# Kernel tuning notes

Measured on AMD Instinct MI355X. Metric: run time of the kernel, lower is better.

The kernel has to match this reference:

```python
import jax, jax.numpy as jnp
import numpy as np

B, T, H, A = 16, 6000, 256, 1
NOTE_CLS = 104            # note_num + 4
NOTE_NUM, NOTE_START = 100, 30
THRESHOLD = 0.5
MIN_GAP = 9


def conv1d(x, w, b):
    # x: [B,T,C], w: [K,Cin,Cout] (kernel 3, padding 1 == SAME)
    return jax.lax.conv_general_dilated(x, w, (1,), 'SAME', dimension_numbers=('NWC', 'WIO', 'NWC')) + b


def layer_norm(x, g, b, eps=1e-5):
    m = jnp.mean(x, -1, keepdims=True)
    v = jnp.mean((x - m) ** 2, -1, keepdims=True)
    return (x - m) * jax.lax.rsqrt(v + eps) * g + b


def regulate_boundary(bd_logits, non_padding):
    # threshold -> per-run local argmax -> min-gap NMS merge, sequential per row
    probs = jax.nn.sigmoid(bd_logits)          # [B,T]
    bd = probs > THRESHOLD
    Tn = probs.shape[1]

    def one_row(bd_i, p_i):
        def step(carry, j):
            res, start, last, best_i, best_v = carry
            is_one, pj = bd_i[j], p_i[j]
            opening = is_one & (start < 0)
            # running argmax over current run (first-occurrence tie-break like torch.argmax)
            upd = opening | (is_one & (start >= 0) & (pj > best_v))
            best_i = jnp.where(upd, j, best_i)
            best_v = jnp.where(upd, pj, best_v)
            start = jnp.where(opening, j, start)
            close = (~is_one) & (start >= 0)
            merge = close & ((best_i - last) < MIN_GAP) & (last > 0)
            # Python round() / half-to-even, matches round((bd_idx+last)/2)
            mid = jnp.round((best_i + last).astype(jnp.float32) * 0.5).astype(jnp.int32)
            final_idx = jnp.where(merge, mid, best_i)
            res = res.at[last].set(jnp.where(merge, 0, res[last]))
            res = res.at[final_idx].set(jnp.where(close, 1, res[final_idx]))
            last = jnp.where(close, final_idx, last)
            start = jnp.where(close, jnp.int32(-1), start)
            return (res, start, last, best_i, best_v), None

        init = (jnp.zeros((Tn,), jnp.int32), jnp.int32(-1), jnp.int32(-1), jnp.int32(0), jnp.float32(-1e30))
        (res, *_), _ = jax.lax.scan(step, init, jnp.arange(Tn, dtype=jnp.int32))
        return res

    res = jax.vmap(one_row)(bd, probs)
    res = res.at[:, 0].set(0)
    lens = non_padding.sum(1)                  # bd_res[i, sum(non_padding[i])-1:] = 0
    res = jnp.where(jnp.arange(Tn)[None, :] >= (lens - 1)[:, None], 0, res)
    return res


def setup_inputs() -> dict:
    key = jax.random.key(0)
    ks = jax.random.split(key, 16)
    s = 1.0 / np.sqrt(H)
    return {
        'feat': jax.random.normal(ks[0], (B, T, H), jnp.float32),
        'non_padding': jnp.ones((B, T), jnp.int32),
        'w_bd': jax.random.normal(ks[1], (H, 1), jnp.float32) * s,
        'b_bd': jnp.zeros((1,), jnp.float32),
        'w_attn': jax.random.normal(ks[2], (H, A), jnp.float32) * s,
        'b_attn': jnp.zeros((A,), jnp.float32),
        'conv_w': jax.random.normal(ks[3], (3, H, H), jnp.float32) * s,
        'conv_b': jnp.zeros((H,), jnp.float32),
        'ln_g': jnp.ones((H,), jnp.float32),
        'ln_b': jnp.zeros((H,), jnp.float32),
        'post_w': jax.random.normal(ks[4], (3, H, H), jnp.float32) * s,
        'post_b': jnp.zeros((H,), jnp.float32),
        'w_pitch': jax.random.normal(ks[5], (H, NOTE_CLS), jnp.float32) * s,
        'b_pitch': jnp.zeros((NOTE_CLS,), jnp.float32),
    }


def reference(feat, non_padding, w_bd, b_bd, w_attn, b_attn, conv_w, conv_b, ln_g, ln_b, post_w, post_b, w_pitch, b_pitch):
    # note boundary logits (note_bd_out, temperature 1, clamp)
    note_bd_logits = jnp.clip((feat @ w_bd + b_bd)[..., 0], -16.0, 16.0)      # [B,T]
    note_bd = regulate_boundary(note_bd_logits, non_padding)                  # [B,T] int

    # --- PitchDecoder ---
    attn = jax.nn.sigmoid(feat @ w_attn + b_attn)                             # [B,T,A]
    attn_mean = attn.mean(-1)                                                 # [B,T]
    # mean over heads of feat[...,None]*attn[:,:,None,:] == feat * mean(attn)
    attn_feat = feat * attn_mean[..., None]                                   # [B,T,H]
    mel2note = jnp.cumsum(note_bd, axis=1)                                    # [B,T]
    note_lengths = note_bd.sum(axis=1) + 1
    N = feat.shape[1] + 1                                                     # static upper bound on note_length
    seg = jax.vmap(lambda d, s2: jax.ops.segment_sum(d, s2, num_segments=N))
    denom = seg(attn_mean, mel2note)                                          # [B,N]
    agg = seg(attn_feat, mel2note) / (denom[..., None] + 1e-5)                # [B,N,H]
    # post ConvBlocks (1 residual conv layer + post conv, kernel 3, leakyrelu)
    h = jax.nn.leaky_relu(layer_norm(conv1d(agg, conv_w, conv_b), ln_g, ln_b), 0.01)
    agg = conv1d(agg + h, post_w, post_b)
    note_logits = agg @ w_pitch + b_pitch                                     # [B,N,104]
    note_pred = jnp.argmax(note_logits, axis=-1)
    note_pred = jnp.where((note_pred > NOTE_NUM) | (note_pred < NOTE_START), 0, note_pred)
    return note_bd_logits, note_bd, note_lengths, note_logits, note_pred
```

## Files before the change

kernel.cpp:

```cpp
#include <hip/hip_runtime.h>
#include <math.h>

#define B 16
#define T 6000
#define H 256
#define NPOS 6001
#define NOTE_CLS 104
#define NOTE_NUM 100
#define NOTE_START 30
#define MIN_GAP 9
#define SEGC 384

#define T2 16
#define NT2 ((NPOS + T2 - 1) / T2)
#define CT 8
#define NCT (SEGC / CT)
#define ZSTR 260

#define NWORDS 94
#define MAXRUNS 3088

__global__ __launch_bounds__(256) void k_dots(
    const float* __restrict__ feat,
    const float* __restrict__ w_bd, const float* __restrict__ b_bd,
    const float* __restrict__ w_attn, const float* __restrict__ b_attn,
    float* __restrict__ out_logits, double* __restrict__ dlog,
    float* __restrict__ amean)
{
  int lane = threadIdx.x & 63, wv = threadIdx.x >> 6;
  int row = blockIdx.x * 4 + wv;
  if (row >= B * T) return;
  float4 f  = ((const float4*)(feat + (size_t)row * H))[lane];
  float4 wb = ((const float4*)w_bd)[lane];
  float4 wa = ((const float4*)w_attn)[lane];
  double sb = (double)f.x * wb.x + (double)f.y * wb.y + (double)f.z * wb.z + (double)f.w * wb.w;
  double sa = (double)f.x * wa.x + (double)f.y * wa.y + (double)f.z * wa.z + (double)f.w * wa.w;
  for (int off = 32; off; off >>= 1) { sb += __shfl_down(sb, off); sa += __shfl_down(sa, off); }
  if (lane == 0) {
    double lb = sb + (double)b_bd[0];
    lb = fmin(fmax(lb, -16.0), 16.0);
    out_logits[row] = (float)lb;
    dlog[row] = lb;
    double la = sa + (double)b_attn[0];
    amean[row] = (float)(1.0 / (1.0 + exp(-la)));
  }
}

__device__ __forceinline__ int block_scan_excl(int* a, int n, int tid, int lane,
                                               int wv, int* wsums)
{
  int base = 0;
  for (int c0 = 0; c0 < n; c0 += 256) {
    int i = c0 + tid;
    int v = (i < n) ? a[i] : 0;
    int s = v;
    #pragma unroll
    for (int off = 1; off < 64; off <<= 1) {
      int t = __shfl_up(s, off);
      if (lane >= off) s += t;
    }
    if (lane == 63) wsums[wv] = s;
    __syncthreads();
    int wbase = 0;
    for (int w = 0; w < wv; ++w) wbase += wsums[w];
    int ctot = wsums[0] + wsums[1] + wsums[2] + wsums[3];
    if (i < n) a[i] = base + wbase + s - v;
    base += ctot;
    __syncthreads();
  }
  return base;
}

__global__ __launch_bounds__(256) void k_regulate(
    const double* __restrict__ dlog, const int* __restrict__ non_padding,
    float* __restrict__ out_bd, float* __restrict__ out_len,
    int* __restrict__ seg_start, int* __restrict__ note_len)
{
  __shared__ double row_s[T];
  __shared__ unsigned long long words[96];
  __shared__ unsigned long long smask[NWORDS], emask[NWORDS];
  __shared__ int wcnt[NWORDS], woff[NWORDS], ecnt[NWORDS], eoff[NWORDS];
  __shared__ int starts_s[MAXRUNS];
  __shared__ int ends_s[MAXRUNS];
  __shared__ int besti_s[MAXRUNS];
  __shared__ int cstart_s[MAXRUNS + 1];
  __shared__ int kofs_s[MAXRUNS];
  __shared__ unsigned long long cmask[52];
  __shared__ int ccnt[52], coff[52];
  __shared__ int wsums[4], red_i[4];
  __shared__ int R_s, NC_s, lens_s;

  int b = blockIdx.x, tid = threadIdx.x;
  int lane = tid & 63, wv = tid >> 6;
  const double* row = dlog + (size_t)b * T;

  for (int c = 0; c < 24; ++c) {
    int t = c * 256 + tid;
    double d = (t < T) ? row[t] : -1.0;
    if (t < T) row_s[t] = d;
    unsigned long long m = __ballot((t < T) && (d > 0.0));
    if (lane == 0) words[c * 4 + wv] = m;
  }
  __syncthreads();

  if (tid < NWORDS) {
    unsigned long long bits = words[tid];
    unsigned long long carry = (tid > 0) ? (words[tid - 1] >> 63) : 0ull;
    unsigned long long pm = (bits << 1) | carry;
    unsigned long long sm = bits & ~pm;
    unsigned long long em = (~bits) & pm;
    smask[tid] = sm;  emask[tid] = em;
    wcnt[tid] = __popcll(sm);  ecnt[tid] = __popcll(em);
  }
  __syncthreads();

  if (tid == 0) {
    int a = 0, e = 0;
    #pragma unroll 8
    for (int w = 0; w < NWORDS; ++w) {
      woff[w] = a; a += wcnt[w];
      eoff[w] = e; e += ecnt[w];
    }
    R_s = a;
  }
  __syncthreads();

  if (tid < NWORDS) {
    unsigned long long m = smask[tid];
    int off = woff[tid], base = tid * 64;
    while (m) { int i = __builtin_ctzll(m); starts_s[off++] = base + i; m &= m - 1; }
    m = emask[tid]; off = eoff[tid];
    while (m) { int i = __builtin_ctzll(m); ends_s[off++] = base + i; m &= m - 1; }
  }

  {
    int lens = 0;
    const int* npr = non_padding + (size_t)b * T;
    for (int t = tid; t < T; t += 256) lens += npr[t];
    for (int off = 32; off; off >>= 1) lens += __shfl_down(lens, off);
    if (lane == 0) red_i[wv] = lens;
  }
  __syncthreads();
  if (tid == 0) lens_s = red_i[0] + red_i[1] + red_i[2] + red_i[3];

  int R = R_s;
  int bd_last = (int)((words[(T - 1) >> 6] >> ((T - 1) & 63)) & 1ull);
  int Rc = R - (bd_last ? 1 : 0);

  for (int r = tid; r < R; r += 256) {
    int s = starts_s[r];
    int e = (r < Rc) ? ends_s[r] : T;
    double bv = row_s[s];
    int bi = s;
    for (int t = s + 1; t < e; ++t) {
      double d = row_s[t];
      if (d > bv) { bv = d; bi = t; }
    }
    besti_s[r] = bi;
  }
  __syncthreads();

  int NRW = (Rc + 63) >> 6;
  for (int c0 = 0; c0 < NRW * 64; c0 += 256) {
    int r = c0 + tid;
    bool fl = false;
    if (r < Rc) fl = (r == 0) || (besti_s[r] - besti_s[r - 1] >= MIN_GAP);
    unsigned long long m = __ballot(fl);
    int widx = (c0 >> 6) + wv;
    if (lane == 0 && widx < 52) cmask[widx] = m;
  }
  __syncthreads();
  if (tid < NRW) ccnt[tid] = __popcll(cmask[tid]);
  __syncthreads();
  if (tid == 0) {
    int a = 0;
    for (int w = 0; w < NRW; ++w) { coff[w] = a; a += ccnt[w]; }
    NC_s = a;
  }
  __syncthreads();
  if (tid < NRW) {
    unsigned long long m = cmask[tid];
    int off = coff[tid], base = tid * 64;
    while (m) { int i = __builtin_ctzll(m); cstart_s[off++] = base + i; m &= m - 1; }
  }
  __syncthreads();
  int NC = NC_s;
  if (tid == 0) cstart_s[NC] = Rc;
  __syncthreads();

  for (int j = tid; j < NC; j += 256) {
    int r0 = cstart_s[j], r1 = cstart_s[j + 1];
    int last = -1, kc = 0;
    for (int r = r0; r < r1; ++r) {
      int bi = besti_s[r];
      bool merge = (last > 0) && (bi - last < MIN_GAP);
      int fi = bi;
      if (merge) { int sm2 = bi + last; fi = (sm2 + ((sm2 >> 1) & 1)) >> 1; }
      if (merge) besti_s[r0 + kc - 1] = fi;
      else       besti_s[r0 + kc++]   = fi;
      last = fi;
    }
    kofs_s[j] = kc;
  }
  __syncthreads();

  int K = block_scan_excl(kofs_s, NC, tid, lane, wv, wsums);
  __syncthreads();
  for (int j = tid; j < NC; j += 256) {
    int off = kofs_s[j];
    int cnt = ((j + 1 < NC) ? kofs_s[j + 1] : K) - off;
    int src = cstart_s[j];
    for (int k = 0; k < cnt; ++k) starts_s[off + k] = besti_s[src + k];
  }
  __syncthreads();

  int lens = lens_s;
  for (int i = tid; i < K; i += 256) {
    int e = starts_s[i];
    ends_s[i] = (e != 0 && e < lens - 1) ? 1 : 0;
  }
  __syncthreads();
  int keep = block_scan_excl(ends_s, K, tid, lane, wv, wsums);

  float* obd = out_bd + (size_t)b * T;
  for (int t = tid; t < T; t += 256) obd[t] = 0.f;
  __syncthreads();
  int* ss = seg_start + b * (T + 2);
  for (int i = tid; i < K; i += 256) {
    int e = starts_s[i];
    if (e != 0 && e < lens - 1) {
      int pos = ends_s[i];
      ss[pos + 1] = e;
      obd[e] = 1.f;
    }
  }
  if (tid == 0) {
    ss[0] = 0;
    ss[keep + 1] = T;
    note_len[b] = keep + 1;
    out_len[b] = (float)(keep + 1);
  }
}

__global__ __launch_bounds__(256) void k_consts(
    const float* __restrict__ conv_b, const float* __restrict__ ln_g,
    const float* __restrict__ ln_b, const float* __restrict__ post_w,
    const float* __restrict__ post_b, const float* __restrict__ w_pitch,
    const float* __restrict__ b_pitch,
    float* __restrict__ lmid, float* __restrict__ ledge, int* __restrict__ preds)
{
  __shared__ float hc[H], zm[H], ze[H], red[8];
  __shared__ float lm[NOTE_CLS], le[NOTE_CLS];
  int tid = threadIdx.x, lane = tid & 63, wv = tid >> 6;
  float y = conv_b[tid];
  float s = y;
  for (int off = 32; off; off >>= 1) s += __shfl_down(s, off);
  if (lane == 0) red[wv] = s;
  __syncthreads();
  float mean = (red[0] + red[1] + red[2] + red[3]) * (1.0f / H);
  float d = y - mean, q = d * d;
  for (int off = 32; off; off >>= 1) q += __shfl_down(q, off);
  if (lane == 0) red[4 + wv] = q;
  __syncthreads();
  float var = (red[4] + red[5] + red[6] + red[7]) * (1.0f / H);
  float h = d / sqrtf(var + 1e-5f) * ln_g[tid] + ln_b[tid];
  h = h > 0.f ? h : 0.01f * h;
  hc[tid] = h;
  __syncthreads();
  float am = 0.f, ae = 0.f;
  for (int cin = 0; cin < H; ++cin) {
    float hv = hc[cin];
    float p0 = post_w[(0 * H + cin) * H + tid];
    float p1 = post_w[(1 * H + cin) * H + tid];
    float p2 = post_w[(2 * H + cin) * H + tid];
    am += (p0 + p1 + p2) * hv;
    ae += (p0 + p1) * hv;
  }
  zm[tid] = am + post_b[tid];
  ze[tid] = ae + post_b[tid];
  __syncthreads();
  if (tid < NOTE_CLS) {
    float sm = 0.f, se = 0.f;
    for (int c = 0; c < H; ++c) {
      float w = w_pitch[c * NOTE_CLS + tid];
      sm += zm[c] * w; se += ze[c] * w;
    }
    lm[tid] = sm + b_pitch[tid]; le[tid] = se + b_pitch[tid];
    lmid[tid] = lm[tid]; ledge[tid] = le[tid];
  }
  __syncthreads();
  if (tid == 0) {
    int bi = 0; float bv = lm[0];
    for (int p = 1; p < NOTE_CLS; ++p) if (lm[p] > bv) { bv = lm[p]; bi = p; }
    preds[0] = (bi > NOTE_NUM || bi < NOTE_START) ? 0 : bi;
    bi = 0; bv = le[0];
    for (int p = 1; p < NOTE_CLS; ++p) if (le[p] > bv) { bv = le[p]; bi = p; }
    preds[1] = (bi > NOTE_NUM || bi < NOTE_START) ? 0 : bi;
  }
}

__global__ __launch_bounds__(64) void k_seg(
    const float* __restrict__ feat, const float* __restrict__ amean,
    const int* __restrict__ seg_start, const int* __restrict__ note_len,
    float* __restrict__ agg)
{
  int blk = blockIdx.x;
  int b = blk / SEGC, n = blk - b * SEGC;
  int len = note_len[b];
  int lane = threadIdx.x;
  float4* o4 = (float4*)(agg + ((size_t)b * SEGC + n) * H);
  if (n >= len) {
    if (n < len + 40) o4[lane] = make_float4(0.f, 0.f, 0.f, 0.f);
    return;
  }
  int s = seg_start[b * (T + 2) + n];
  int e = seg_start[b * (T + 2) + n + 1];
  float4 acc = make_float4(0.f, 0.f, 0.f, 0.f);
  float dsum = 0.f;
  for (int t = s; t < e; ++t) {
    float am = amean[(size_t)b * T + t];
    float4 f = ((const float4*)(feat + ((size_t)b * T + t) * H))[lane];
    acc.x += am * f.x; acc.y += am * f.y; acc.z += am * f.z; acc.w += am * f.w;
    dsum += am;
  }
  float dn = dsum + 1e-5f;
  acc.x /= dn; acc.y /= dn; acc.z /= dn; acc.w /= dn;
  o4[lane] = acc;
}

__device__ __forceinline__ void conv_ranges(int len, int& Nz, int& MY)
{
  int t16 = ((len + 2) / 16) * 16;
  if (t16 > SEGC - 16) t16 = SEGC - 16;
  Nz = t16 + 16;
  MY = Nz + 2;
  if (MY > NPOS) MY = NPOS;
}

__global__ __launch_bounds__(256) void k_conv1u(
    const float* __restrict__ agg,
    const float* __restrict__ conv_w, const float* __restrict__ conv_b,
    const float* __restrict__ ln_g, const float* __restrict__ ln_b,
    const int* __restrict__ note_len,
    float* __restrict__ u_buf)
{
  int blk = blockIdx.x;
  int b = blk / NCT, tile = blk - b * NCT;
  int t0 = tile * CT;
  int len = note_len[b];
  int Nz, MY;
  conv_ranges(len, Nz, MY);
  if (t0 >= MY) return;

  __shared__ float xs[H][12];
  __shared__ float rs_[CT][4], rq_[CT][4];
  __shared__ float smean[CT], srstd[CT];

  int tid = threadIdx.x;
  int lane = tid & 63, wv = tid >> 6;
  const float* aggb = agg + (size_t)b * SEGC * H;

  #pragma unroll
  for (int r = 0; r < 10; ++r) {
    int p = t0 - 1 + r;
    float v = 0.f;
    if (p >= 0 && p < SEGC) v = aggb[(size_t)p * H + tid];
    xs[tid][r] = v;
  }
  if (tid < H) { xs[tid][10] = 0.f; xs[tid][11] = 0.f; }
  __syncthreads();

  float acc[CT];
  #pragma unroll
  for (int j = 0; j < CT; ++j) acc[j] = 0.f;
  #pragma unroll 4
  for (int cin = 0; cin < H; ++cin) {
    float w0 = conv_w[cin * H + tid];
    float w1 = conv_w[(H + cin) * H + tid];
    float w2 = conv_w[(2 * H + cin) * H + tid];
    float4 X = *(const float4*)&xs[cin][0];
    float4 Y = *(const float4*)&xs[cin][4];
    float4 Z = *(const float4*)&xs[cin][8];
    float L[10] = { X.x, X.y, X.z, X.w, Y.x, Y.y, Y.z, Y.w, Z.x, Z.y };
    #pragma unroll
    for (int j = 0; j < CT; ++j)
      acc[j] += w0 * L[j] + w1 * L[j + 1] + w2 * L[j + 2];
  }
  {
    float cb = conv_b[tid];
    #pragma unroll
    for (int j = 0; j < CT; ++j) acc[j] += cb;
  }

  #pragma unroll 1
  for (int j = 0; j < CT; ++j) {
    float s = acc[j], q = acc[j] * acc[j];
    for (int off = 32; off; off >>= 1) { s += __shfl_down(s, off); q += __shfl_down(q, off); }
    if (lane == 0) { rs_[j][wv] = s; rq_[j][wv] = q; }
  }
  __syncthreads();
  if (tid < CT) {
    float S = rs_[tid][0] + rs_[tid][1] + rs_[tid][2] + rs_[tid][3];
    float Q = rq_[tid][0] + rq_[tid][1] + rq_[tid][2] + rq_[tid][3];
    float mean = S * (1.0f / H);
    float var = Q * (1.0f / H) - mean * mean;
    if (var < 0.f) var = 0.f;
    smean[tid] = mean;
    srstd[tid] = 1.0f / sqrtf(var + 1e-5f);
  }
  __syncthreads();

  float g = ln_g[tid], bb = ln_b[tid];
  float* ub = u_buf + (size_t)b * SEGC * H;
  #pragma unroll
  for (int j = 0; j < CT; ++j) {
    int m = t0 + j;
    if (m < MY) {
      float h = (acc[j] - smean[j]) * srstd[j] * g + bb;
      h = h > 0.f ? h : 0.01f * h;
      ub[(size_t)m * H + tid] = xs[tid][j + 1] + h;
    }
  }
}

__global__ __launch_bounds__(256) void k_conv2p(
    const float* __restrict__ u_buf,
    const float* __restrict__ post_w, const float* __restrict__ post_b,
    const float* __restrict__ w_pitch, const float* __restrict__ b_pitch,
    const int* __restrict__ note_len,
    float* __restrict__ out3, float* __restrict__ out4)
{
  int blk = blockIdx.x;
  int b = blk / NCT, tile = blk - b * NCT;
  int t0 = tile * CT;
  int len = note_len[b];
  if ((t0 & ~15) > len + 2) return;
  int Nz, MY;
  conv_ranges(len, Nz, MY);

  __shared__ float us_[H][12];
  __shared__ float zt[CT * ZSTR];
  __shared__ float pvs[CT][26];
  __shared__ int   pis[CT][26];

  int tid = threadIdx.x;
  const float* ub = u_buf + (size_t)b * SEGC * H;

  #pragma unroll
  for (int r = 0; r < 10; ++r) {
    int m = t0 - 1 + r;
    float v = 0.f;
    if (m >= 0 && m < MY) v = ub[(size_t)m * H + tid];
    us_[tid][r] = v;
  }
  if (tid < H) { us_[tid][10] = 0.f; us_[tid][11] = 0.f; }
  __syncthreads();

  float acc[CT];
  #pragma unroll
  for (int j = 0; j < CT; ++j) acc[j] = 0.f;
  #pragma unroll 4
  for (int cin = 0; cin < H; ++cin) {
    float w0 = post_w[cin * H + tid];
    float w1 = post_w[(H + cin) * H + tid];
    float w2 = post_w[(2 * H + cin) * H + tid];
    float4 X = *(const float4*)&us_[cin][0];
    float4 Y = *(const float4*)&us_[cin][4];
    float4 Z = *(const float4*)&us_[cin][8];
    float L[10] = { X.x, X.y, X.z, X.w, Y.x, Y.y, Y.z, Y.w, Z.x, Z.y };
    #pragma unroll
    for (int j = 0; j < CT; ++j)
      acc[j] += w0 * L[j] + w1 * L[j + 1] + w2 * L[j + 2];
  }
  {
    float pb = post_b[tid];
    #pragma unroll
    for (int j = 0; j < CT; ++j) zt[j * ZSTR + tid] = acc[j] + pb;
  }
  __syncthreads();

  if (tid < 208) {
    int n8 = tid / 26, c26 = tid - n8 * 26;
    float4 a = make_float4(0.f, 0.f, 0.f, 0.f);
    const float* z = &zt[n8 * ZSTR];
    #pragma unroll 4
    for (int cin = 0; cin < H; ++cin) {
      float4 w4 = *(const float4*)&w_pitch[cin * NOTE_CLS + 4 * c26];
      float zv = z[cin];
      a.x += zv * w4.x; a.y += zv * w4.y; a.z += zv * w4.z; a.w += zv * w4.w;
    }
    float4 bp = *(const float4*)&b_pitch[4 * c26];
    a.x += bp.x; a.y += bp.y; a.z += bp.z; a.w += bp.w;
    int n = t0 + n8;
    if (n < NPOS)
      *(float4*)&out3[((size_t)b * NPOS + n) * NOTE_CLS + 4 * c26] = a;
    float bv = a.x; int bi = 4 * c26;
    if (a.y > bv) { bv = a.y; bi = 4 * c26 + 1; }
    if (a.z > bv) { bv = a.z; bi = 4 * c26 + 2; }
    if (a.w > bv) { bv = a.w; bi = 4 * c26 + 3; }
    pvs[n8][c26] = bv; pis[n8][c26] = bi;
  }
  __syncthreads();
  if (tid < CT && t0 + tid < NPOS) {
    float bv = pvs[tid][0]; int bi = pis[tid][0];
    #pragma unroll 1
    for (int k = 1; k < 26; ++k)
      if (pvs[tid][k] > bv) { bv = pvs[tid][k]; bi = pis[tid][k]; }
    int pred = (bi > NOTE_NUM || bi < NOTE_START) ? 0 : bi;
    out4[(size_t)b * NPOS + t0 + tid] = (float)pred;
  }
}

__global__ __launch_bounds__(256) void k_tail(
    const float* __restrict__ lmid, const float* __restrict__ ledge,
    const int* __restrict__ preds, const int* __restrict__ note_len,
    float* __restrict__ out3, float* __restrict__ out4)
{
  int blk = blockIdx.x;
  int b = blk / NT2, tile = blk - b * NT2;
  int t0 = tile * T2;
  int len = note_len[b];
  if (t0 <= len + 2) return;
  __shared__ float lm[NOTE_CLS], le[NOTE_CLS];
  int tid = threadIdx.x;
  if (tid < NOTE_CLS) { lm[tid] = lmid[tid]; le[tid] = ledge[tid]; }
  __syncthreads();
  int pm = preds[0], pe = preds[1];
  for (int i = tid; i < T2 * NOTE_CLS; i += 256) {
    int dn = i / NOTE_CLS;
    int n = t0 + dn, p = i - dn * NOTE_CLS;
    if (n >= NPOS) continue;
    out3[((size_t)b * NPOS + n) * NOTE_CLS + p] = (n == NPOS - 1) ? le[p] : lm[p];
  }
  if (tid < T2) {
    int n = t0 + tid;
    if (n < NPOS) out4[(size_t)b * NPOS + n] = (float)((n == NPOS - 1) ? pe : pm);
  }
}

extern "C" void kernel_launch(void* const* d_in, const int* in_sizes, int n_in,
                              void* d_out, int out_size, void* d_ws, size_t ws_size,
                              hipStream_t stream) {
  (void)in_sizes; (void)n_in; (void)out_size; (void)ws_size;
  const float* feat    = (const float*)d_in[0];
  const int*   nonpad  = (const int*)d_in[1];
  const float* w_bd    = (const float*)d_in[2];
  const float* b_bd    = (const float*)d_in[3];
  const float* w_attn  = (const float*)d_in[4];
  const float* b_attn  = (const float*)d_in[5];
  const float* conv_w  = (const float*)d_in[6];
  const float* conv_b  = (const float*)d_in[7];
  const float* ln_g    = (const float*)d_in[8];
  const float* ln_b    = (const float*)d_in[9];
  const float* post_w  = (const float*)d_in[10];
  const float* post_b  = (const float*)d_in[11];
  const float* w_pitch = (const float*)d_in[12];
  const float* b_pitch = (const float*)d_in[13];

  float* out  = (float*)d_out;
  float* out0 = out;
  float* out1 = out + (size_t)B * T;
  float* out2 = out + 2ull * B * T;
  float* out3 = out2 + B;
  float* out4 = out3 + (size_t)B * NPOS * NOTE_CLS;

  char* ws = (char*)d_ws;
  double* dlog  = (double*)(ws + 0);
  float*  amean = (float*)(ws + 768000);
  int*    segst = (int*)(ws + 1152000);
  int*    nlen  = (int*)(ws + 1536128);
  float*  lmid  = (float*)(ws + 1536192);
  float*  ledge = (float*)(ws + 1536608);
  int*    preds = (int*)(ws + 1537024);
  float*  agg   = (float*)(ws + 1537536);
  float*  u_buf = (float*)(ws + 1537536 + 6291456);

  k_dots<<<(B * T) / 4, 256, 0, stream>>>(feat, w_bd, b_bd, w_attn, b_attn, out0, dlog, amean);
  k_regulate<<<B, 256, 0, stream>>>(dlog, nonpad, out1, out2, segst, nlen);
  k_consts<<<1, 256, 0, stream>>>(conv_b, ln_g, ln_b, post_w, post_b, w_pitch, b_pitch, lmid, ledge, preds);
  k_seg<<<B * SEGC, 64, 0, stream>>>(feat, amean, segst, nlen, agg);
  k_conv1u<<<B * NCT, 256, 0, stream>>>(agg, conv_w, conv_b, ln_g, ln_b, nlen, u_buf);
  k_conv2p<<<B * NCT, 256, 0, stream>>>(u_buf, post_w, post_b, w_pitch, b_pitch, nlen, out3, out4);
  k_tail<<<B * NT2, 256, 0, stream>>>(lmid, ledge, preds, nlen, out3, out4);
}
```

Before: 295.9 us.

## Split conv input channels across two thread halves with shared-memory reduction

The two conv kernels now launch 512 threads per block. Each half of the block handles 128 of the 256 input channels, and the partial sums are reduced through shared memory. The pitch projection is spread over 416 threads using float2 instead of 208 threads using float4. The intent is more parallelism and latency hiding per block on the short sequential conv loop, at the cost of extra shared memory, an extra barrier, and half the threads idling during the layer norm and epilogue. MY is also clamped to SEGC.

After: 314.1 us. 1.06x slower.

```diff
diff --git a/kernel.cpp b/kernel.cpp
--- a/kernel.cpp
+++ b/kernel.cpp
@@ -335,9 +335,10 @@
   Nz = t16 + 16;
   MY = Nz + 2;
   if (MY > NPOS) MY = NPOS;
-}
-
-__global__ __launch_bounds__(256) void k_conv1u(
+  if (MY > SEGC) MY = SEGC;
+}
+
+__global__ __launch_bounds__(512) void k_conv1u(
     const float* __restrict__ agg,
     const float* __restrict__ conv_w, const float* __restrict__ conv_b,
     const float* __restrict__ ln_g, const float* __restrict__ ln_b,
@@ -353,50 +354,63 @@
   if (t0 >= MY) return;
 
   __shared__ float xs[H][12];
+  __shared__ float psum[2][CT][ZSTR];
   __shared__ float rs_[CT][4], rq_[CT][4];
   __shared__ float smean[CT], srstd[CT];
 
   int tid = threadIdx.x;
-  int lane = tid & 63, wv = tid >> 6;
+  int cout = tid & 255, ch = tid >> 8;
+  int lane = tid & 63;
   const float* aggb = agg + (size_t)b * SEGC * H;
 
   #pragma unroll
-  for (int r = 0; r < 10; ++r) {
+  for (int i = 0; i < 5; ++i) {
+    int r = ch * 5 + i;
     int p = t0 - 1 + r;
     float v = 0.f;
-    if (p >= 0 && p < SEGC) v = aggb[(size_t)p * H + tid];
-    xs[tid][r] = v;
-  }
-  if (tid < H) { xs[tid][10] = 0.f; xs[tid][11] = 0.f; }
+    if (p >= 0 && p < SEGC) v = aggb[(size_t)p * H + cout];
+    xs[cout][r] = v;
+  }
+  if (ch == 0) { xs[cout][10] = 0.f; xs[cout][11] = 0.f; }
   __syncthreads();
 
   float acc[CT];
   #pragma unroll
   for (int j = 0; j < CT; ++j) acc[j] = 0.f;
-  #pragma unroll 4
-  for (int cin = 0; cin < H; ++cin) {
-    float w0 = conv_w[cin * H + tid];
-    float w1 = conv_w[(H + cin) * H + tid];
-    float w2 = conv_w[(2 * H + cin) * H + tid];
-    float4 X = *(const float4*)&xs[cin][0];
-    float4 Y = *(const float4*)&xs[cin][4];
-    float4 Z = *(const float4*)&xs[cin][8];
-    float L[10] = { X.x, X.y, X.z, X.w, Y.x, Y.y, Y.z, Y.w, Z.x, Z.y };
+  {
+    int cbase = ch * 128;
+    #pragma unroll 4
+    for (int ci = 0; ci < 128; ++ci) {
+      int cin = cbase + ci;
+      float w0 = conv_w[cin * H + cout];
+      float w1 = conv_w[(H + cin) * H + cout];
+      float w2 = conv_w[(2 * H + cin) * H + cout];
+      float4 X = *(const float4*)&xs[cin][0];
+      float4 Y = *(const float4*)&xs[cin][4];
+      float4 Z = *(const float4*)&xs[cin][8];
+      float L[10] = { X.x, X.y, X.z, X.w, Y.x, Y.y, Y.z, Y.w, Z.x, Z.y };
+      #pragma unroll
+      for (int j = 0; j < CT; ++j)
+        acc[j] += w0 * L[j] + w1 * L[j + 1] + w2 * L[j + 2];
+    }
+  }
+  #pragma unroll
+  for (int j = 0; j < CT; ++j) psum[ch][j][cout] = acc[j];
+  __syncthreads();
+
+  float y[CT];
+  if (ch == 0) {
+    float cb = conv_b[cout];
+    int wv4 = tid >> 6;
     #pragma unroll
     for (int j = 0; j < CT; ++j)
-      acc[j] += w0 * L[j] + w1 * L[j + 1] + w2 * L[j + 2];
-  }
-  {
-    float cb = conv_b[tid];
-    #pragma unroll
-    for (int j = 0; j < CT; ++j) acc[j] += cb;
-  }
-
-  #pragma unroll 1
-  for (int j = 0; j < CT; ++j) {
-    float s = acc[j], q = acc[j] * acc[j];
-    for (int off = 32; off; off >>= 1) { s += __shfl_down(s, off); q += __shfl_down(q, off); }
-    if (lane == 0) { rs_[j][wv] = s; rq_[j][wv] = q; }
+      y[j] = psum[0][j][cout] + psum[1][j][cout] + cb;
+    #pragma unroll 1
+    for (int j = 0; j < CT; ++j) {
+      float s = y[j], q = y[j] * y[j];
+      for (int off = 32; off; off >>= 1) { s += __shfl_down(s, off); q += __shfl_down(q, off); }
+      if (lane == 0) { rs_[j][wv4] = s; rq_[j][wv4] = q; }
+    }
   }
   __syncthreads();
   if (tid < CT) {
@@ -410,20 +424,22 @@
   }
   __syncthreads();
 
-  float g = ln_g[tid], bb = ln_b[tid];
-  float* ub = u_buf + (size_t)b * SEGC * H;
-  #pragma unroll
-  for (int j = 0; j < CT; ++j) {
-    int m = t0 + j;
-    if (m < MY) {
-      float h = (acc[j] - smean[j]) * srstd[j] * g + bb;
-      h = h > 0.f ? h : 0.01f * h;
-      ub[(size_t)m * H + tid] = xs[tid][j + 1] + h;
-    }
-  }
-}
-
-__global__ __launch_bounds__(256) void k_conv2p(
+  if (ch == 0) {
+    float g = ln_g[cout], bb = ln_b[cout];
+    float* ub = u_buf + (size_t)b * SEGC * H;
+    #pragma unroll
+    for (int j = 0; j < CT; ++j) {
+      int m = t0 + j;
+      if (m < MY) {
+        float h = (y[j] - smean[j]) * srstd[j] * g + bb;
+        h = h > 0.f ? h : 0.01f * h;
+        ub[(size_t)m * H + cout] = xs[cout][j + 1] + h;
+      }
+    }
+  }
+}
+
+__global__ __launch_bounds__(512) void k_conv2p(
     const float* __restrict__ u_buf,
     const float* __restrict__ post_w, const float* __restrict__ post_b,
     const float* __restrict__ w_pitch, const float* __restrict__ b_pitch,
@@ -439,72 +455,84 @@
   conv_ranges(len, Nz, MY);
 
   __shared__ float us_[H][12];
+  __shared__ float psum[2][CT][ZSTR];
   __shared__ float zt[CT * ZSTR];
-  __shared__ float pvs[CT][26];
-  __shared__ int   pis[CT][26];
+  __shared__ float pvs[CT][52];
+  __shared__ int   pis[CT][52];
 
   int tid = threadIdx.x;
+  int cout = tid & 255, ch = tid >> 8;
   const float* ub = u_buf + (size_t)b * SEGC * H;
 
   #pragma unroll
-  for (int r = 0; r < 10; ++r) {
+  for (int i = 0; i < 5; ++i) {
+    int r = ch * 5 + i;
     int m = t0 - 1 + r;
     float v = 0.f;
-    if (m >= 0 && m < MY) v = ub[(size_t)m * H + tid];
-    us_[tid][r] = v;
-  }
-  if (tid < H) { us_[tid][10] = 0.f; us_[tid][11] = 0.f; }
+    if (m >= 0 && m < MY) v = ub[(size_t)m * H + cout];
+    us_[cout][r] = v;
+  }
+  if (ch == 0) { us_[cout][10] = 0.f; us_[cout][11] = 0.f; }
   __syncthreads();
 
   float acc[CT];
   #pragma unroll
   for (int j = 0; j < CT; ++j) acc[j] = 0.f;
-  #pragma unroll 4
-  for (int cin = 0; cin < H; ++cin) {
-    float w0 = post_w[cin * H + tid];
-    float w1 = post_w[(H + cin) * H + tid];
-    float w2 = post_w[(2 * H + cin) * H + tid];
-    float4 X = *(const float4*)&us_[cin][0];
-    float4 Y = *(const float4*)&us_[cin][4];
-    float4 Z = *(const float4*)&us_[cin][8];
-    float L[10] = { X.x, X.y, X.z, X.w, Y.x, Y.y, Y.z, Y.w, Z.x, Z.y };
+  {
+    int cbase = ch * 128;
+    #pragma unroll 4
+    for (int ci = 0; ci < 128; ++ci) {
+      int cin = cbase + ci;
+      float w0 = post_w[cin * H + cout];
+      float w1 = post_w[(H + cin) * H + cout];
+      float w2 = post_w[(2 * H + cin) * H + cout];
+      float4 X = *(const float4*)&us_[cin][0];
+      float4 Y = *(const float4*)&us_[cin][4];
+      float4 Z = *(const float4*)&us_[cin][8];
+      float L[10] = { X.x, X.y, X.z, X.w, Y.x, Y.y, Y.z, Y.w, Z.x, Z.y };
+      #pragma unroll
+      for (int j = 0; j < CT; ++j)
+        acc[j] += w0 * L[j] + w1 * L[j + 1] + w2 * L[j + 2];
+    }
+  }
+  #pragma unroll
+  for (int j = 0; j < CT; ++j) psum[ch][j][cout] = acc[j];
+  __syncthreads();
+
+  if (ch == 0) {
+    float pb = post_b[cout];
     #pragma unroll
     for (int j = 0; j < CT; ++j)
-      acc[j] += w0 * L[j] + w1 * L[j + 1] + w2 * L[j + 2];
-  }
-  {
-    float pb = post_b[tid];
-    #pragma unroll
-    for (int j = 0; j < CT; ++j) zt[j * ZSTR + tid] = acc[j] + pb;
-  }
-  __syncthreads();
-
-  if (tid < 208) {
-    int n8 = tid / 26, c26 = tid - n8 * 26;
-    float4 a = make_float4(0.f, 0.f, 0.f, 0.f);
+      zt[j * ZSTR + cout] = psum[0][j][cout] + psum[1][j][cout] + pb;
+  }
+  __syncthreads();
+
+  if (tid < 416) {
+    int n8 = tid / 52, c52 = tid - n8 * 52;
+    float ax = 0.f, ay = 0.f;
     const float* z = &zt[n8 * ZSTR];
     #pragma unroll 4
     for (int cin = 0; cin < H; ++cin) {
-      float4 w4 = *(const float4*)&w_pitch[cin * NOTE_CLS + 4 * c26];
+      float2 w2 = *(const float2*)&w_pitch[cin * NOTE_CLS + 2 * c52];
       float zv = z[cin];
-      a.x += zv * w4.x; a.y += zv * w4.y; a.z += zv * w4.z; a.w += zv * w4.w;
-    }
-    float4 bp = *(const float4*)&b_pitch[4 * c26];
-    a.x += bp.x; a.y += bp.y; a.z += bp.z; a.w += bp.w;
+      ax += zv * w2.x; ay += zv * w2.y;
+    }
+    float2 bp = *(const float2*)&b_pitch[2 * c52];
+    ax += bp.x; ay += bp.y;
     int n = t0 + n8;
-    if (n < NPOS)
-      *(float4*)&out3[((size_t)b * NPOS + n) * NOTE_CLS + 4 * c26] = a;
-    float bv = a.x; int bi = 4 * c26;
-    if (a.y > bv) { bv = a.y; bi = 4 * c26 + 1; }
-    if (a.z > bv) { bv = a.z; bi = 4 * c26 + 2; }
-    if (a.w > bv) { bv = a.w; bi = 4 * c26 + 3; }
-    pvs[n8][c26] = bv; pis[n8][c26] = bi;
+    if (n < NPOS) {
+      float2 o; o.x = ax; o.y = ay;
+      *(float2*)&out3[((size_t)b * NPOS + n) * NOTE_CLS + 2 * c52] = o;
+    }
+    float bv = ax; int bi = 2 * c52;
+    if (ay > bv) { bv = ay; bi = 2 * c52 + 1; }
+    pvs[n8][c52] = bv; pis[n8][c52] = bi;
   }
   __syncthreads();
   if (tid < CT && t0 + tid < NPOS) {
     float bv = pvs[tid][0]; int bi = pis[tid][0];
     #pragma unroll 1
-    for (int k = 1; k < 26; ++k)
+    for (int k = 1; k < 52; ++k)
       if (pvs[tid][k] > bv) { bv = pvs[tid][k]; bi = pis[tid][k]; }
     int pred = (bi > NOTE_NUM || bi < NOTE_START) ? 0 : bi;
     out4[(size_t)b * NPOS + t0 + tid] = (float)pred;
@@ -579,7 +607,7 @@
   k_regulate<<<B, 256, 0, stream>>>(dlog, nonpad, out1, out2, segst, nlen);
   k_consts<<<1, 256, 0, stream>>>(conv_b, ln_g, ln_b, post_w, post_b, w_pitch, b_pitch, lmid, ledge, preds);
   k_seg<<<B * SEGC, 64, 0, stream>>>(feat, amean, segst, nlen, agg);
-  k_conv1u<<<B * NCT, 256, 0, stream>>>(agg, conv_w, conv_b, ln_g, ln_b, nlen, u_buf);
-  k_conv2p<<<B * NCT, 256, 0, stream>>>(u_buf, post_w, post_b, w_pitch, b_pitch, nlen, out3, out4);
+  k_conv1u<<<B * NCT, 512, 0, stream>>>(agg, conv_w, conv_b, ln_g, ln_b, nlen, u_buf);
+  k_conv2p<<<B * NCT, 512, 0, stream>>>(u_buf, post_w, post_b, w_pitch, b_pitch, nlen, out3, out4);
   k_tail<<<B * NT2, 256, 0, stream>>>(lmid, ledge, preds, nlen, out3, out4);
 }
```
